# Kernel tuning notes

Measured on AMD Instinct MI355X. Metric: run time of the kernel, lower is better.

## Reference

```python
import jax, jax.numpy as jnp
import numpy as np
from jax import lax

B = 32768
INPUT_SIZE = 42  # 1 rocket_y + 20*(rock_x, rock_y) + 1 speed
H, W = 10, 15    # grid_height, grid_width
OUT = 3


def setup_inputs() -> dict:
    key = jax.random.key(0)
    ks = jax.random.split(key, 8)
    p = lambda k, s: (jax.random.normal(k, s) * 0.05).astype(jnp.float32)
    x = (jax.random.uniform(ks[0], (B, INPUT_SIZE)) * 16.0).astype(jnp.float32)
    return {
        "x": x,
        "conv1_w": p(ks[1], (16, 2, 3, 3)), "conv1_b": jnp.zeros((16,), jnp.float32),
        "conv2_w": p(ks[2], (32, 16, 3, 3)), "conv2_b": jnp.zeros((32,), jnp.float32),
        "fc1_w": p(ks[3], (32 * H * W + 1, 256)), "fc1_b": jnp.zeros((256,), jnp.float32),
        "fc2_w": p(ks[4], (256, 128)), "fc2_b": jnp.zeros((128,), jnp.float32),
        "fc3_w": p(ks[5], (128, OUT)), "fc3_b": jnp.zeros((OUT,), jnp.float32),
    }


def _conv(h, w, b):
    # 3x3, stride 1, padding 1 (SAME), NCHW / OIHW
    return lax.conv_general_dilated(h, w, (1, 1), "SAME",
                                    dimension_numbers=("NCHW", "OIHW", "NCHW")) \
           + b[None, :, None, None]


def _build_grid(x):
    """Vectorized replacement of the per-sample Python scatter loop."""
    bsz = x.shape[0]
    b = jnp.arange(bsz)
    dt = x.dtype
    # rocket channel: grid[i, rocket_y, 1] = 1 if 0 <= rocket_y < H
    ry = x[:, 0].astype(jnp.int32)
    rv = ((ry >= 0) & (ry < H)).astype(dt)
    rocket = jnp.zeros((bsz, H, W), dt).at[b, jnp.clip(ry, 0, H - 1), 1].add(rv)
    # rock channel: pairs (x, y) at columns (1,2),(3,4),...,(39,40)
    kx = x[:, 1:INPUT_SIZE - 1:2].astype(jnp.int32)  # [B, 20]
    ky = x[:, 2:INPUT_SIZE - 1:2].astype(jnp.int32)  # [B, 20]
    kv = ((kx >= 0) & (ky >= 0) & (kx < W) & (ky < H)).astype(dt)
    rock = jnp.zeros((bsz, H, W), dt).at[
        b[:, None], jnp.clip(ky, 0, H - 1), jnp.clip(kx, 0, W - 1)
    ].max(kv)  # set-to-1 semantics (duplicates ok)
    return jnp.stack([rocket, rock], axis=1)  # [B, 2, H, W]


def reference(x, conv1_w, conv1_b, conv2_w, conv2_b,
              fc1_w, fc1_b, fc2_w, fc2_b, fc3_w, fc3_b):
    grid = _build_grid(x)
    h = jax.nn.relu(_conv(grid, conv1_w, conv1_b))
    h = jax.nn.relu(_conv(h, conv2_w, conv2_b))
    h = h.reshape(x.shape[0], -1)                      # NCHW flatten, matches torch .view
    h = jnp.concatenate([h, x[:, -1:]], axis=1)        # append speed
    h = jax.nn.relu(h @ fc1_w + fc1_b)
    h = jax.nn.relu(h @ fc2_w + fc2_b)
    return h @ fc3_w + fc3_b
```

## Files before the change

kernel.cpp:

```cpp
#include <hip/hip_runtime.h>
#include <hip/hip_bf16.h>
#include <stdint.h>

typedef short short8 __attribute__((ext_vector_type(8)));
typedef float f32x4  __attribute__((ext_vector_type(4)));

__device__ __forceinline__ uint16_t f2bf(float f) {
    union { float f; uint32_t u; } v; v.f = f;
    return (uint16_t)((v.u + 0x7FFFu + ((v.u >> 16) & 1u)) >> 16);
}
__device__ __forceinline__ float bf2f(uint16_t h) {
    union { uint32_t u; float f; } v; v.u = ((uint32_t)h) << 16;
    return v.f;
}
__device__ __forceinline__ void gl_lds16(const void* g, void* l) {
    __builtin_amdgcn_global_load_lds(
        (const __attribute__((address_space(1))) unsigned int*)g,
        (__attribute__((address_space(3))) unsigned int*)l, 16, 0, 0);
}

#define NSAMP_TOT 32768
#define H2_PER_S  5120

__global__ void repack_all(const float* __restrict__ f1w, const float* __restrict__ c2w,
                           const float* __restrict__ c1w, const float* __restrict__ f2w,
                           uint16_t* __restrict__ w1pt, uint16_t* __restrict__ w2rt,
                           uint16_t* __restrict__ w1rt, uint16_t* __restrict__ w2bt) {
    int tid = threadIdx.x, b = blockIdx.x;
    if (b < 160) {
        int f_s = b >> 4, cp = b & 15, n = tid;
        __align__(16) uint16_t vals[32];
        #pragma unroll
        for (int o = 0; o < 32; o++) {
            int c = cp * 2 + (o >> 4), pl = o & 15;
            int p = f_s * 16 + pl;
            float v = (p < 150) ? f1w[(size_t)(c * 150 + p) * 256 + n] : 0.f;
            vals[o] = f2bf(v);
        }
        int win = f_s * 8 + (cp >> 1);
        size_t rowbase = (size_t)n * H2_PER_S + win * 64;
        #pragma unroll
        for (int j = 0; j < 4; j++) {
            int qlog = (cp * 4 + j) & 7;
            int qphy = qlog ^ (n & 7);
            *(uint4*)&w1pt[rowbase + qphy * 8] = *(uint4*)&vals[j * 8];
        }
    } else if (b == 160) {
        for (int t = tid; t < 32 * 160; t += 256) {
            int n = t / 160, k = t % 160;
            float v = 0.f;
            if (k < 144) {
                int tap = k >> 4, ci = k & 15, dy = tap / 3, dx = tap % 3;
                v = c2w[((n * 16 + ci) * 3 + dy) * 3 + dx];
            }
            w2rt[t] = f2bf(v);
        }
        for (int t = tid; t < 16 * 32; t += 256) {
            int n = t >> 5, k = t & 31;
            float v = 0.f;
            if (k < 18) {
                int tap = k >> 1, ch = k & 1;
                int dy = (tap * 11) >> 5, dx = tap - dy * 3;
                v = c1w[((n * 2 + ch) * 3 + dy) * 3 + dx];
            }
            w1rt[t] = f2bf(v);
        }
    } else {
        __shared__ float tr2[32][129];
        int kb = b - 161;
        for (int i = tid; i < 32 * 128; i += 256) {
            int kk = i >> 7, n = i & 127;
            tr2[kk][n] = f2w[(size_t)(kb * 32 + kk) * 128 + n];
        }
        __syncthreads();
        int n = tid >> 1, half = tid & 1;
        __align__(16) uint16_t tmp[16];
        #pragma unroll
        for (int q = 0; q < 16; q++) tmp[q] = f2bf(tr2[half * 16 + q][n]);
        *(uint4*)&w2bt[(size_t)n * 256 + kb * 32 + half * 16]     = *(uint4*)&tmp[0];
        *(uint4*)&w2bt[(size_t)n * 256 + kb * 32 + half * 16 + 8] = *(uint4*)&tmp[8];
    }
}

__launch_bounds__(512, 2)
__global__ void k12_fused(const float* __restrict__ x, const uint16_t* __restrict__ w1rt,
                          const float* __restrict__ c1b, const uint16_t* __restrict__ w2rt,
                          const float* __restrict__ c2b, uint16_t* __restrict__ h2, int s0) {
    __shared__ float sx[8 * 42];
    __shared__ __align__(16) uint16_t grd[8 * 204 * 2];
    __shared__ __align__(16) uint16_t h1s[8 * 204 * 16];
    int tid = threadIdx.x;
    int w = tid >> 6, l = tid & 63, lr = l & 15, lk = l >> 4;

    short8 b1f = *(const short8*)&w1rt[lr * 32 + lk * 8];
    short8 bfr[5][2];
    #pragma unroll
    for (int ks = 0; ks < 5; ks++)
        #pragma unroll
        for (int nf = 0; nf < 2; nf++)
            bfr[ks][nf] = *(const short8*)&w2rt[(nf * 16 + lr) * 160 + ks * 32 + lk * 8];
    float cb1r = c1b[lr];
    float cb0 = c2b[lr], cb1 = c2b[16 + lr];

    uint4 z4 = make_uint4(0, 0, 0, 0);
    for (int i = tid; i < 3672; i += 512) {
        if (i < 408) ((uint4*)grd)[i] = z4;
        else         ((uint4*)h1s)[i - 408] = z4;
    }
    int sbase = s0 + blockIdx.x * 8;
    for (int i = tid; i < 8 * 42; i += 512) sx[i] = x[(size_t)(sbase + i / 42) * 42 + (i % 42)];
    __syncthreads();

    if (tid < 160) {
        int sl = tid / 20, r = tid % 20;
        int kx = (int)sx[sl * 42 + 1 + 2 * r];
        int ky = (int)sx[sl * 42 + 2 + 2 * r];
        if (kx >= 0 && kx < 15 && ky >= 0 && ky < 10)
            grd[(sl * 204 + (ky + 1) * 17 + (kx + 1)) * 2 + 1] = 0x3F80;
    } else if (tid < 168) {
        int sl = tid - 160;
        int ry = (int)sx[sl * 42];
        if (ry >= 0 && ry < 10)
            grd[(sl * 204 + (ry + 1) * 17 + 2) * 2 + 0] = 0x3F80;
    }
    __syncthreads();

    for (int f = w; f < 75; f += 8) {
        int rA = f * 16 + lr;
        int sA = rA / 150, pA = rA - sA * 150;
        int y = pA / 15, xx = pA - y * 15;
        int base = sA * 204 + y * 17 + xx;
        union { uint32_t d[4]; short8 s; } au;
        #pragma unroll
        for (int jj = 0; jj < 4; jj++) {
            int t = lk * 4 + jj;
            int valid = t < 9;
            int tc = valid ? t : 0;
            int dy = (tc * 11) >> 5, dx = tc - dy * 3;
            uint32_t v = *(const uint32_t*)&grd[(base + dy * 17 + dx) * 2];
            au.d[jj] = valid ? v : 0u;
        }
        f32x4 acc = {};
        acc = __builtin_amdgcn_mfma_f32_16x16x32_bf16(au.s, b1f, acc, 0, 0, 0);
        #pragma unroll
        for (int j = 0; j < 4; j++) {
            int row = f * 16 + lk * 4 + j;
            int s2 = row / 150, p2 = row - s2 * 150;
            int y2 = p2 / 15, x2 = p2 - y2 * 15;
            float v = acc[j] + cb1r;
            h1s[(s2 * 204 + (y2 + 1) * 17 + (x2 + 1)) * 16 + lr] = f2bf(v > 0.f ? v : 0.f);
        }
    }
    __syncthreads();

    short8 zz = {0, 0, 0, 0, 0, 0, 0, 0};
    for (int f = w; f < 80; f += 8) {
        int s_local = f / 10, f_s = f - s_local * 10;
        int p160 = f_s * 16 + lr;
        int pA = p160 < 150 ? p160 : 0;
        int y = pA / 15, xx = pA - y * 15;
        f32x4 acc0 = {}, acc1 = {};
        #pragma unroll
        for (int ks = 0; ks < 5; ks++) {
            int idx = ks * 4 + lk;
            int idc = idx < 18 ? idx : 0;
            int tap = idc >> 1, half = idc & 1;
            int dy = (tap * 11) >> 5, dx = tap - dy * 3;
            short8 av = *(const short8*)&h1s[((s_local * 204 + (y + dy) * 17 + (xx + dx)) * 16) + half * 8];
            av = idx < 18 ? av : zz;
            acc0 = __builtin_amdgcn_mfma_f32_16x16x32_bf16(av, bfr[ks][0], acc0, 0, 0, 0);
            acc1 = __builtin_amdgcn_mfma_f32_16x16x32_bf16(av, bfr[ks][1], acc1, 0, 0, 0);
        }
        ushort4 v0, v1;
        { float a = acc0[0] + cb0; v0.x = f2bf(a > 0.f ? a : 0.f); }
        { float a = acc0[1] + cb0; v0.y = f2bf(a > 0.f ? a : 0.f); }
        { float a = acc0[2] + cb0; v0.z = f2bf(a > 0.f ? a : 0.f); }
        { float a = acc0[3] + cb0; v0.w = f2bf(a > 0.f ? a : 0.f); }
        { float a = acc1[0] + cb1; v1.x = f2bf(a > 0.f ? a : 0.f); }
        { float a = acc1[1] + cb1; v1.y = f2bf(a > 0.f ? a : 0.f); }
        { float a = acc1[2] + cb1; v1.z = f2bf(a > 0.f ? a : 0.f); }
        { float a = acc1[3] + cb1; v1.w = f2bf(a > 0.f ? a : 0.f); }
        int k0 = f_s * 512 + lr * 16 + lk * 4;
        int k0s = (k0 & ~63) | (((((k0 >> 3) & 7) ^ s_local)) << 3) | (k0 & 7);
        int k1 = k0 + 256;
        int k1s = (k1 & ~63) | (((((k1 >> 3) & 7) ^ s_local)) << 3) | (k1 & 7);
        size_t sb = (size_t)(blockIdx.x * 8 + s_local) * H2_PER_S;
        *(ushort4*)&h2[sb + k0s] = v0;
        *(ushort4*)&h2[sb + k1s] = v1;
    }
}

__launch_bounds__(256)
__global__ void k3_fused(const uint16_t* __restrict__ h2, const uint16_t* __restrict__ w1pt,
                         const float* __restrict__ f1b, const float* __restrict__ f1w,
                         const float* __restrict__ x, const uint16_t* __restrict__ w2bt,
                         const float* __restrict__ f2b, const float* __restrict__ f3w,
                         const float* __restrict__ f3b, float* __restrict__ out, int s0) {
    __shared__ __align__(16) uint16_t uLDS[(32 + 256) * 64];
    uint16_t* lA = uLDS;
    uint16_t* lB = uLDS + 32 * 64;
    uint16_t* lH = uLDS;
    __shared__ float sbias[256], swl[256], sspeed[32], sb2[128], sw3[384];
    __shared__ float pf[4][32][3];
    int tid = threadIdx.x;
    int bm = blockIdx.x;
    sbias[tid] = f1b[tid];
    swl[tid]   = f1w[(size_t)4800 * 256 + tid];
    if (tid < 32)  sspeed[tid] = x[(size_t)(s0 + bm * 32 + tid) * 42 + 41];
    if (tid >= 64 && tid < 192) sb2[tid - 64] = f2b[tid - 64];
    for (int i = tid; i < 384; i += 256) sw3[i] = f3w[i];

    int w = tid >> 6, l = tid & 63, lr = l & 15, lk = l >> 4;
    const uint16_t* ga = &h2[(size_t)(bm * 32 + (tid >> 3)) * H2_PER_S + (tid & 7) * 8];
    uint16_t* la_ = lA + tid * 8;
    const uint16_t* gb[8]; uint16_t* lb_[8];
    #pragma unroll
    for (int i = 0; i < 8; i++) {
        int c2 = tid + i * 256;
        gb[i] = &w1pt[(size_t)(c2 >> 3) * H2_PER_S + (c2 & 7) * 8];
        lb_[i] = lB + c2 * 8;
    }
    int aoff[2][2], boff[4][2];
    #pragma unroll
    for (int ks = 0; ks < 2; ks++) {
        int cl = (ks * 4 + lk);
        #pragma unroll
        for (int mf = 0; mf < 2; mf++)
            aoff[mf][ks] = (mf * 16 + lr) * 64 + ((cl ^ (lr & 7)) << 3);
        #pragma unroll
        for (int nf = 0; nf < 4; nf++)
            boff[nf][ks] = (w * 64 + nf * 16 + lr) * 64 + ((cl ^ (lr & 7)) << 3);
    }

    f32x4 acc[2][4] = {};
    for (int kt = 0; kt < 80; kt++) {
        gl_lds16(ga, la_); ga += 64;
        #pragma unroll
        for (int i = 0; i < 8; i++) { gl_lds16(gb[i], lb_[i]); gb[i] += 64; }
        __syncthreads();
        #pragma unroll
        for (int ks = 0; ks < 2; ks++) {
            short8 a[2], b[4];
            #pragma unroll
            for (int mf = 0; mf < 2; mf++)
                a[mf] = *(const short8*)&lA[aoff[mf][ks]];
            #pragma unroll
            for (int nf = 0; nf < 4; nf++)
                b[nf] = *(const short8*)&lB[boff[nf][ks]];
            #pragma unroll
            for (int mf = 0; mf < 2; mf++)
                #pragma unroll
                for (int nf = 0; nf < 4; nf++)
                    acc[mf][nf] = __builtin_amdgcn_mfma_f32_16x16x32_bf16(a[mf], b[nf], acc[mf][nf], 0, 0, 0);
        }
        __syncthreads();
    }
    #pragma unroll
    for (int mf = 0; mf < 2; mf++) {
        #pragma unroll
        for (int j = 0; j < 4; j++) {
            int r = mf * 16 + lk * 4 + j;
            float sp = sspeed[r];
            #pragma unroll
            for (int nf = 0; nf < 4; nf++) {
                int col = w * 64 + nf * 16 + lr;
                float v = acc[mf][nf][j] + sbias[col] + sp * swl[col];
                int cc = col >> 3, cl = col & 7;
                lH[r * 256 + ((cc ^ (r & 7)) << 3) + cl] = f2bf(v > 0.f ? v : 0.f);
            }
        }
    }
    __syncthreads();
    f32x4 acc2[2][2] = {};
    #pragma unroll
    for (int ks2 = 0; ks2 < 8; ks2++) {
        short8 a2[2], bv[2];
        #pragma unroll
        for (int mf2 = 0; mf2 < 2; mf2++) {
            int row = mf2 * 16 + lr;
            int chunk = (ks2 * 4 + lk) ^ (row & 7);
            a2[mf2] = *(const short8*)&lH[row * 256 + chunk * 8];
        }
        #pragma unroll
        for (int nf2 = 0; nf2 < 2; nf2++)
            bv[nf2] = *(const short8*)&w2bt[(size_t)(w * 32 + nf2 * 16 + lr) * 256 + ks2 * 32 + lk * 8];
        #pragma unroll
        for (int mf2 = 0; mf2 < 2; mf2++)
            #pragma unroll
            for (int nf2 = 0; nf2 < 2; nf2++)
                acc2[mf2][nf2] = __builtin_amdgcn_mfma_f32_16x16x32_bf16(a2[mf2], bv[nf2], acc2[mf2][nf2], 0, 0, 0);
    }
    float p3[2][4][3];
    #pragma unroll
    for (int mf2 = 0; mf2 < 2; mf2++)
        #pragma unroll
        for (int j = 0; j < 4; j++)
            #pragma unroll
            for (int o = 0; o < 3; o++) p3[mf2][j][o] = 0.f;
    #pragma unroll
    for (int mf2 = 0; mf2 < 2; mf2++) {
        #pragma unroll
        for (int nf2 = 0; nf2 < 2; nf2++) {
            int col = w * 32 + nf2 * 16 + lr;
            float w0 = sw3[col * 3 + 0], w1v = sw3[col * 3 + 1], w2v = sw3[col * 3 + 2];
            #pragma unroll
            for (int j = 0; j < 4; j++) {
                float v = acc2[mf2][nf2][j] + sb2[col];
                v = v > 0.f ? v : 0.f;
                p3[mf2][j][0] += v * w0;
                p3[mf2][j][1] += v * w1v;
                p3[mf2][j][2] += v * w2v;
            }
        }
    }
    #pragma unroll
    for (int off = 1; off < 16; off <<= 1)
        #pragma unroll
        for (int mf2 = 0; mf2 < 2; mf2++)
            #pragma unroll
            for (int j = 0; j < 4; j++)
                #pragma unroll
                for (int o = 0; o < 3; o++)
                    p3[mf2][j][o] += __shfl_xor(p3[mf2][j][o], off);
    if (lr == 0) {
        #pragma unroll
        for (int mf2 = 0; mf2 < 2; mf2++)
            #pragma unroll
            for (int j = 0; j < 4; j++) {
                int r = mf2 * 16 + lk * 4 + j;
                #pragma unroll
                for (int o = 0; o < 3; o++) pf[w][r][o] = p3[mf2][j][o];
            }
    }
    __syncthreads();
    if (tid < 96) {
        int r = tid / 3, o = tid - r * 3;
        out[(size_t)(s0 + bm * 32 + r) * 3 + o] =
            pf[0][r][o] + pf[1][r][o] + pf[2][r][o] + pf[3][r][o] + f3b[o];
    }
}

extern "C" void kernel_launch(void* const* d_in, const int* in_sizes, int n_in,
                              void* d_out, int out_size, void* d_ws, size_t ws_size,
                              hipStream_t stream) {
    const float* x   = (const float*)d_in[0];
    const float* c1w = (const float*)d_in[1];
    const float* c1b = (const float*)d_in[2];
    const float* c2w = (const float*)d_in[3];
    const float* c2b = (const float*)d_in[4];
    const float* f1w = (const float*)d_in[5];
    const float* f1b = (const float*)d_in[6];
    const float* f2w = (const float*)d_in[7];
    const float* f2b = (const float*)d_in[8];
    const float* f3w = (const float*)d_in[9];
    const float* f3b = (const float*)d_in[10];
    float* out = (float*)d_out;

    char* ws = (char*)d_ws;
    uint16_t* w1pt = (uint16_t*)ws;
    uint16_t* w2rt = (uint16_t*)(ws + 2621440);
    uint16_t* w2bt = (uint16_t*)(ws + 2631680);
    uint16_t* w1rt = (uint16_t*)(ws + 2697216);
    size_t base = 2698240;

    int chunk = NSAMP_TOT;
    while (chunk > 128 && base + (size_t)chunk * 10240 > ws_size) chunk >>= 1;
    uint16_t* h2 = (uint16_t*)(ws + base);

    repack_all<<<169, 256, 0, stream>>>(f1w, c2w, c1w, f2w, w1pt, w2rt, w1rt, w2bt);

    for (int s0 = 0; s0 < NSAMP_TOT; s0 += chunk) {
        k12_fused<<<chunk / 8, 512, 0, stream>>>(x, w1rt, c1b, w2rt, c2b, h2, s0);
        k3_fused<<<chunk / 32, 256, 0, stream>>>(h2, w1pt, f1b, f1w, x, w2bt, f2b, f3w, f3b, out, s0);
    }
}
```

Measured before the change: 305.0 us.

## Double-buffer LDS tiles in fused FC kernel to overlap loads with MFMA

Makes the fc1 GEMM main loop in k3_fused use two LDS buffers. The next K-tile's global-to-LDS loads are issued before the MFMAs on the current tile, and the barrier that used to follow the load issue is removed. The aim is to hide global load latency behind matrix compute. In exchange, the LDS footprint roughly doubles, which can cut resident blocks per CU. The barrier that closes each iteration still waits for the outstanding loads, so the overlap is limited to one tile's compute.

```diff
diff --git a/kernel.cpp b/kernel.cpp
--- a/kernel.cpp
+++ b/kernel.cpp
@@ -196,9 +196,8 @@
                          const float* __restrict__ x, const uint16_t* __restrict__ w2bt,
                          const float* __restrict__ f2b, const float* __restrict__ f3w,
                          const float* __restrict__ f3b, float* __restrict__ out, int s0) {
-    __shared__ __align__(16) uint16_t uLDS[(32 + 256) * 64];
-    uint16_t* lA = uLDS;
-    uint16_t* lB = uLDS + 32 * 64;
+    #define BUF_E (32 * 64 + 256 * 64)
+    __shared__ __align__(16) uint16_t uLDS[2 * BUF_E];
     uint16_t* lH = uLDS;
     __shared__ float sbias[256], swl[256], sspeed[32], sb2[128], sw3[384];
     __shared__ float pf[4][32][3];
@@ -212,13 +211,19 @@
 
     int w = tid >> 6, l = tid & 63, lr = l & 15, lk = l >> 4;
     const uint16_t* ga = &h2[(size_t)(bm * 32 + (tid >> 3)) * H2_PER_S + (tid & 7) * 8];
-    uint16_t* la_ = lA + tid * 8;
-    const uint16_t* gb[8]; uint16_t* lb_[8];
+    const uint16_t* gb[8];
     #pragma unroll
     for (int i = 0; i < 8; i++) {
         int c2 = tid + i * 256;
         gb[i] = &w1pt[(size_t)(c2 >> 3) * H2_PER_S + (c2 & 7) * 8];
-        lb_[i] = lB + c2 * 8;
+    }
+    uint16_t* laD[2]; uint16_t* lbD[2][8];
+    #pragma unroll
+    for (int bb = 0; bb < 2; bb++) {
+        laD[bb] = uLDS + bb * BUF_E + tid * 8;
+        #pragma unroll
+        for (int i = 0; i < 8; i++)
+            lbD[bb][i] = uLDS + bb * BUF_E + 2048 + (tid + i * 256) * 8;
     }
     int aoff[2][2], boff[4][2];
     #pragma unroll
@@ -229,24 +234,31 @@
             aoff[mf][ks] = (mf * 16 + lr) * 64 + ((cl ^ (lr & 7)) << 3);
         #pragma unroll
         for (int nf = 0; nf < 4; nf++)
-            boff[nf][ks] = (w * 64 + nf * 16 + lr) * 64 + ((cl ^ (lr & 7)) << 3);
+            boff[nf][ks] = 2048 + (w * 64 + nf * 16 + lr) * 64 + ((cl ^ (lr & 7)) << 3);
     }
 
     f32x4 acc[2][4] = {};
+    gl_lds16(ga, laD[0]); ga += 64;
+    #pragma unroll
+    for (int i = 0; i < 8; i++) { gl_lds16(gb[i], lbD[0][i]); gb[i] += 64; }
+    __syncthreads();
     for (int kt = 0; kt < 80; kt++) {
-        gl_lds16(ga, la_); ga += 64;
-        #pragma unroll
-        for (int i = 0; i < 8; i++) { gl_lds16(gb[i], lb_[i]); gb[i] += 64; }
-        __syncthreads();
+        int cur = kt & 1;
+        if (kt < 79) {
+            gl_lds16(ga, laD[cur ^ 1]); ga += 64;
+            #pragma unroll
+            for (int i = 0; i < 8; i++) { gl_lds16(gb[i], lbD[cur ^ 1][i]); gb[i] += 64; }
+        }
+        const uint16_t* buf = uLDS + cur * BUF_E;
         #pragma unroll
         for (int ks = 0; ks < 2; ks++) {
             short8 a[2], b[4];
             #pragma unroll
             for (int mf = 0; mf < 2; mf++)
-                a[mf] = *(const short8*)&lA[aoff[mf][ks]];
+                a[mf] = *(const short8*)&buf[aoff[mf][ks]];
             #pragma unroll
             for (int nf = 0; nf < 4; nf++)
-                b[nf] = *(const short8*)&lB[boff[nf][ks]];
+                b[nf] = *(const short8*)&buf[boff[nf][ks]];
             #pragma unroll
             for (int mf = 0; mf < 2; mf++)
                 #pragma unroll
@@ -338,6 +350,7 @@
         out[(size_t)(s0 + bm * 32 + r) * 3 + o] =
             pf[0][r][o] + pf[1][r][o] + pf[2][r][o] + pf[3][r][o] + f3b[o];
     }
+    #undef BUF_E
 }
 
 extern "C" void kernel_launch(void* const* d_in, const int* in_sizes, int n_in,
```

After: 300.9 us. No clear change (-1.4%).
